# Optimization experiments

Measured on AMD Instinct MI355X. Metric: run time of the kernel, lower is better.

Reference implementation:

```python
import jax, jax.numpy as jnp
import numpy as np

B, D, L = 4096, 128, 4
ALPHA = 1.0
SLOPE = 0.1  # LeakyReLU negative slope


def _leaky(h):
    return jnp.where(h > 0, h, SLOPE * h)


def _dleaky(h):
    return jnp.where(h > 0, 1.0, SLOPE).astype(h.dtype)


def setup_inputs() -> dict:
    key = jax.random.key(0)
    ks = jax.random.split(key, 7)
    scale = 0.5 / np.sqrt(D)  # keep residual roughly Lipschitz < 1
    x = jax.random.normal(ks[0], (B, D), jnp.float32)
    W1 = jax.random.normal(ks[1], (L, D, D), jnp.float32) * scale
    b1 = jax.random.normal(ks[2], (L, D), jnp.float32) * 0.01
    W2 = jax.random.normal(ks[3], (L, D, D), jnp.float32) * scale
    b2 = jax.random.normal(ks[4], (L, D), jnp.float32) * 0.01
    W3 = jax.random.normal(ks[5], (L, D, D), jnp.float32) * scale
    b3 = jax.random.normal(ks[6], (L, D), jnp.float32) * 0.01
    return {"x": x, "W1": W1, "b1": b1, "W2": W2, "b2": b2, "W3": W3, "b3": b3}


def reference(x, W1, b1, W2, b2, W3, b3):
    logdet = jnp.zeros(x.shape[0], x.dtype)
    for i in range(L):  # small fixed number of structurally distinct blocks
        w1, w2, w3 = W1[i], W2[i], W3[i]
        # --- block forward: x <- x + alpha * f(x) ---
        h1 = x @ w1.T + b1[i]
        h2 = _leaky(h1) @ w2.T + b2[i]
        f = _leaky(h2) @ w3.T + b3[i]
        x = x + ALPHA * f
        # --- log|det J_f| evaluated at the NEW x (as in the original code) ---
        g1 = x @ w1.T + b1[i]          # [B, D] pre-activation 1
        d1 = _dleaky(g1)
        g2 = _leaky(g1) @ w2.T + b2[i]  # [B, D] pre-activation 2
        d2 = _dleaky(g2)
        # J[b] = w3 @ diag(d2[b]) @ w2 @ diag(d1[b]) @ w1  -> [B, D, D]
        J = (w3[None, :, :] * d2[:, None, :]) @ w2
        J = (J * d1[:, None, :]) @ w1
        s = jnp.linalg.svd(J, compute_uv=False)  # [B, D] singular values
        logdet = logdet + jnp.sum(jnp.log(s), axis=-1)
    return x, logdet
```

## Files before the change

kernel.cpp:

```cpp
#include <hip/hip_runtime.h>

typedef __attribute__((ext_vector_type(8))) short short8;
typedef __attribute__((ext_vector_type(4))) float float4f;

#define PITCH 136
#define ROWS 32
#define LOG_SLOPE -2.302585092994046f
#define LN2 0.6931471805599453f
#define NBLK 140
#define LDS_BYTES 69760
#define WS_BIAS 4160
#define WS_WPLANES 8192
#define NWELEM 196608

__device__ __forceinline__ float bf2f(unsigned int u) {
    return __builtin_bit_cast(float, u << 16);
}
__device__ __forceinline__ unsigned short f2bf(float f) {
    unsigned int x = __builtin_bit_cast(unsigned int, f);
    x += 0x7fff + ((x >> 16) & 1);
    return (unsigned short)(x >> 16);
}
__device__ __forceinline__ float4f vmsub(float4f a, float s, float4f b) {
    a[0] -= s * b[0]; a[1] -= s * b[1]; a[2] -= s * b[2]; a[3] -= s * b[3];
    return a;
}

template<int ISF32>
__device__ __forceinline__ float ldv(const void* p, int i) {
    if (ISF32) return ((const float*)p)[i];
    return bf2f(((const unsigned short*)p)[i]);
}

__device__ __forceinline__ int detect_f32(const unsigned short* W1u, int lane) {
    unsigned int u = W1u[lane * 2];
    unsigned int e = (u >> 7) & 0xFF;
    int bad = (e < 64) || (e > 135);
    return __ballot(bad) != 0ull;
}

__device__ __forceinline__ float4f mfma16(short8 a, short8 b, float4f c) {
    return __builtin_amdgcn_mfma_f32_16x16x32_bf16(a, b, c, 0, 0, 0);
}

__device__ __forceinline__ void split8(float4f a, float4f b, short8& hi, short8& lo) {
#pragma unroll
    for (int j = 0; j < 4; ++j) {
        float v = a[j]; unsigned short h = f2bf(v);
        hi[j] = (short)h; lo[j] = (short)f2bf(v - bf2f(h));
        v = b[j]; h = f2bf(v);
        hi[4 + j] = (short)h; lo[4 + j] = (short)f2bf(v - bf2f(h));
    }
}

__global__ void k_prep(const void* __restrict__ W1, const void* __restrict__ W2,
                       const void* __restrict__ W3, const void* __restrict__ b1,
                       const void* __restrict__ b2, const void* __restrict__ b3,
                       float* __restrict__ ws) {
    const int tid = threadIdx.x, bid = blockIdx.x;
    const int isf32 = detect_f32((const unsigned short*)W1, tid & 63);
    unsigned short* whi = (unsigned short*)(ws + WS_WPLANES);
    unsigned short* wlo = whi + NWELEM;
    if (bid < 96) {
        int s = (bid * 256 + tid) * 8;
        int mat = s >> 14, off = s & 16383;
        int wsel = mat >> 2;
        const void* Wm = wsel == 0 ? W1 : (wsel == 1 ? W2 : W3);
        int src = (mat & 3) * 16384 + off;
        short8 hi, lo;
        if (isf32) {
            const float* p = (const float*)Wm + src;
            split8(*(const float4f*)p, *(const float4f*)(p + 4), hi, lo);
        } else {
            hi = *(const short8*)((const unsigned short*)Wm + src);
            lo = (short8){0, 0, 0, 0, 0, 0, 0, 0};
        }
        *(short8*)(whi + s) = hi;
        *(short8*)(wlo + s) = lo;
    } else {
        for (int e = tid; e < 1536; e += 256) {
            int bsel = e >> 9, idx = e & 511;
            const void* bp = bsel == 0 ? b1 : (bsel == 1 ? b2 : b3);
            ws[WS_BIAS + e] = isf32 ? ((const float*)bp)[idx]
                                    : bf2f(((const unsigned short*)bp)[idx]);
        }
        if (tid == 0) ((int*)ws)[0] = 0;
    }
}

struct W8 { short8 v[16]; };

__device__ __forceinline__ W8 loadW(const unsigned short* __restrict__ wh,
                                    const unsigned short* __restrict__ wl,
                                    int c0, int c1, int q) {
    W8 r;
#pragma unroll
    for (int kk = 0; kk < 4; ++kk) {
        const int kc = kk * 32 + q * 8;
        r.v[kk * 4 + 0] = *(const short8*)(wh + c0 * 128 + kc);
        r.v[kk * 4 + 1] = *(const short8*)(wh + c1 * 128 + kc);
        r.v[kk * 4 + 2] = *(const short8*)(wl + c0 * 128 + kc);
        r.v[kk * 4 + 3] = *(const short8*)(wl + c1 * 128 + kc);
    }
    return r;
}

template<int MODE>
__device__ __forceinline__ W8 matvec(const W8& w,
        const unsigned short* inh, const unsigned short* inl,
        unsigned short* outh, unsigned short* outl,
        const unsigned short* resh, const unsigned short* resl,
        const unsigned short* __restrict__ nwh, const unsigned short* __restrict__ nwl,
        const float* __restrict__ bias,
        int lane, int colb, int* cnt) {
    const int m = lane & 15, q = lane >> 4;
    const int c0 = colb + m, c1 = colb + 16 + m;
    float b0 = bias[c0], b1v = bias[c1];
    float4f acc[2][2];
#pragma unroll
    for (int rt = 0; rt < 2; ++rt) {
        acc[rt][0] = (float4f){b0, b0, b0, b0};
        acc[rt][1] = (float4f){b1v, b1v, b1v, b1v};
    }
    __syncthreads();
    W8 wn = loadW(nwh, nwl, c0, c1, q);
#pragma unroll
    for (int kk = 0; kk < 4; ++kk) {
        const int kc = kk * 32 + q * 8;
#pragma unroll
        for (int rt = 0; rt < 2; ++rt) {
            short8 xh = *(const short8*)(inh + (rt * 16 + m) * PITCH + kc);
            short8 xl = *(const short8*)(inl + (rt * 16 + m) * PITCH + kc);
            acc[rt][0] = mfma16(xh, w.v[kk * 4 + 0], acc[rt][0]);
            acc[rt][0] = mfma16(xl, w.v[kk * 4 + 0], acc[rt][0]);
            acc[rt][0] = mfma16(xh, w.v[kk * 4 + 2], acc[rt][0]);
            acc[rt][1] = mfma16(xh, w.v[kk * 4 + 1], acc[rt][1]);
            acc[rt][1] = mfma16(xl, w.v[kk * 4 + 1], acc[rt][1]);
            acc[rt][1] = mfma16(xh, w.v[kk * 4 + 3], acc[rt][1]);
        }
    }
    int c[2][4];
#pragma unroll
    for (int rt = 0; rt < 2; ++rt) {
#pragma unroll
        for (int r = 0; r < 4; ++r) {
            float v0 = acc[rt][0][r], v1 = acc[rt][1][r];
            int row = rt * 16 + q * 4 + r;
            int o0 = row * PITCH + c0, o1 = row * PITCH + c1;
            if (MODE == 1) {
                v0 += bf2f(resh[o0]) + bf2f(resl[o0]);
                v1 += bf2f(resh[o1]) + bf2f(resl[o1]);
            }
            if (MODE >= 2) c[rt][r] = (v0 <= 0.0f) + (v1 <= 0.0f);
            if (MODE == 0 || MODE == 2) {
                v0 = v0 > 0.0f ? v0 : 0.1f * v0;
                v1 = v1 > 0.0f ? v1 : 0.1f * v1;
            }
            if (MODE != 3) {
                unsigned short h0 = f2bf(v0);
                outh[o0] = h0; outl[o0] = f2bf(v0 - bf2f(h0));
                unsigned short h1 = f2bf(v1);
                outh[o1] = h1; outl[o1] = f2bf(v1 - bf2f(h1));
            }
        }
    }
    if (MODE >= 2) {
#pragma unroll
        for (int rt = 0; rt < 2; ++rt) {
#pragma unroll
            for (int r = 0; r < 4; ++r) {
                int cc = c[rt][r];
                cc += __shfl_xor(cc, 1);
                cc += __shfl_xor(cc, 2);
                cc += __shfl_xor(cc, 4);
                cc += __shfl_xor(cc, 8);
                if (m == 0) atomicAdd(&cnt[rt * 16 + q * 4 + r], cc);
            }
        }
    }
    return wn;
}

template<int ISF32>
__device__ __forceinline__ void fwd(int bid, int tid, int lane, char* ldsb,
                                    const void* x, const float* ws, void* out,
                                    float* wsw) {
    unsigned short* P = (unsigned short*)ldsb;
    unsigned short* Ah = P;
    unsigned short* Al = P + 1 * ROWS * PITCH;
    unsigned short* Bh = P + 2 * ROWS * PITCH;
    unsigned short* Bl = P + 3 * ROWS * PITCH;
    unsigned short* Th = P + 4 * ROWS * PITCH;
    unsigned short* Tl = P + 5 * ROWS * PITCH;
    unsigned short* Uh = P + 6 * ROWS * PITCH;
    unsigned short* Ul = P + 7 * ROWS * PITCH;
    int* cnt = (int*)(P + 8 * ROWS * PITCH);
    const unsigned short* whi = (const unsigned short*)(ws + WS_WPLANES);
    const unsigned short* wlo = whi + NWELEM;
    const float* bias = ws + WS_BIAS;
    const int r0 = bid * ROWS;
    const int m = lane & 15, q = lane >> 4;
    const int colb = (tid >> 6) * 32;
    const int c0 = colb + m, c1 = colb + 16 + m;
    W8 wcur = loadW(whi, wlo, c0, c1, q);
    for (int e = tid; e < ROWS * 128; e += 256) {
        int r = e >> 7, c = e & 127;
        float v = ldv<ISF32>(x, (r0 + r) * 128 + c);
        unsigned short h = f2bf(v);
        Ah[r * PITCH + c] = h;
        Al[r * PITCH + c] = f2bf(v - bf2f(h));
    }
    if (tid < ROWS) cnt[tid] = 0;
    unsigned short *curh = Ah, *curl = Al, *othh = Bh, *othl = Bl;
#pragma unroll 1
    for (int layer = 0; layer < 4; ++layer) {
        const unsigned short* w1h = whi + (0 + layer) * 16384;
        const unsigned short* w1l = wlo + (0 + layer) * 16384;
        const unsigned short* w2h = whi + (4 + layer) * 16384;
        const unsigned short* w2l = wlo + (4 + layer) * 16384;
        const unsigned short* w3h = whi + (8 + layer) * 16384;
        const unsigned short* w3l = wlo + (8 + layer) * 16384;
        const unsigned short* n1h = whi + ((layer + 1) & 3) * 16384;
        const unsigned short* n1l = wlo + ((layer + 1) & 3) * 16384;
        const float* b1p = bias + layer * 128;
        const float* b2p = bias + 512 + layer * 128;
        const float* b3p = bias + 1024 + layer * 128;
        wcur = matvec<0>(wcur, curh, curl, Th, Tl, 0, 0, w2h, w2l, b1p, lane, colb, cnt);
        wcur = matvec<0>(wcur, Th, Tl, Uh, Ul, 0, 0, w3h, w3l, b2p, lane, colb, cnt);
        wcur = matvec<1>(wcur, Uh, Ul, othh, othl, curh, curl, w1h, w1l, b3p, lane, colb, cnt);
        wcur = matvec<2>(wcur, othh, othl, Th, Tl, 0, 0, w2h, w2l, b1p, lane, colb, cnt);
        wcur = matvec<3>(wcur, Th, Tl, Th, Tl, 0, 0, n1h, n1l, b2p, lane, colb, cnt);
        unsigned short* t;
        t = curh; curh = othh; othh = t;
        t = curl; curl = othl; othl = t;
    }
    __syncthreads();
    for (int e = tid; e < ROWS * 128; e += 256) {
        int r = e >> 7, c = e & 127;
        float v = bf2f(curh[r * PITCH + c]) + bf2f(curl[r * PITCH + c]);
        if (ISF32) ((float*)out)[(r0 + r) * 128 + c] = v;
        else ((unsigned short*)out)[(r0 + r) * 128 + c] = f2bf(v);
    }
    if (tid < ROWS) wsw[64 + r0 + tid] = (float)cnt[tid];
}

template<int ISF32>
__device__ __forceinline__ float lu_logdet(int id, int tid, float* lds,
        const void* W1, const void* W2, const void* W3) {
    const int wsel = id % 3;
    const void* Wm = (wsel == 0 ? W1 : (wsel == 1 ? W2 : W3));
    const int ofs = (id / 3) * 16384;
    const int tx = tid & 31, ty = tid >> 5;
    float* rowbuf = lds;
    float* colbuf = lds + 1024;
    float4f V[16];
#pragma unroll
    for (int m = 0; m < 16; ++m) {
        int base = ofs + (ty + 8 * m) * 128 + 4 * tx;
        if (ISF32) {
            V[m] = *(const float4f*)((const float*)Wm + base);
        } else {
            ushort4 u = *(const ushort4*)((const unsigned short*)Wm + base);
            V[m] = (float4f){bf2f(u.x), bf2f(u.y), bf2f(u.z), bf2f(u.w)};
        }
    }
    if (ty < 4) *(float4f*)&rowbuf[ty * 128 + 4 * tx] = V[0];
    if (tx == 0) {
#pragma unroll
        for (int j = 0; j < 4; ++j) {
#pragma unroll
            for (int mg = 0; mg < 4; ++mg) {
                float4f t = {V[mg * 4 + 0][j], V[mg * 4 + 1][j],
                             V[mg * 4 + 2][j], V[mg * 4 + 3][j]};
                *(float4f*)&colbuf[j * 128 + ty * 16 + mg * 4] = t;
            }
        }
    }
    __syncthreads();
    float logacc = 0.0f;
#pragma unroll 1
    for (int kap = 0; kap < 32; ++kap) {
        const int K = kap * 4;
        const int buf = (kap & 1) * 512;
        float4f D[4], R[4], C[4][4];
#pragma unroll
        for (int j = 0; j < 4; ++j) {
            D[j] = *(const float4f*)&rowbuf[buf + j * 128 + K];
            R[j] = *(const float4f*)&rowbuf[buf + j * 128 + 4 * tx];
#pragma unroll
            for (int mg = 0; mg < 4; ++mg)
                C[j][mg] = *(const float4f*)&colbuf[buf + j * 128 + ty * 16 + mg * 4];
        }
        float p0 = D[0][0], i0 = 1.0f / p0;
        float l10 = D[1][0] * i0, l20 = D[2][0] * i0, l30 = D[3][0] * i0;
        D[1] = vmsub(D[1], l10, D[0]); R[1] = vmsub(R[1], l10, R[0]);
        D[2] = vmsub(D[2], l20, D[0]); R[2] = vmsub(R[2], l20, R[0]);
        D[3] = vmsub(D[3], l30, D[0]); R[3] = vmsub(R[3], l30, R[0]);
        float p1 = D[1][1], i1 = 1.0f / p1;
        float l21 = D[2][1] * i1, l31 = D[3][1] * i1;
        D[2] = vmsub(D[2], l21, D[1]); R[2] = vmsub(R[2], l21, R[1]);
        D[3] = vmsub(D[3], l31, D[1]); R[3] = vmsub(R[3], l31, R[1]);
        float p2 = D[2][2], i2 = 1.0f / p2;
        float l32 = D[3][2] * i2;
        D[3] = vmsub(D[3], l32, D[2]); R[3] = vmsub(R[3], l32, R[2]);
        float p3 = D[3][3], i3 = 1.0f / p3;
        logacc += __log2f(fabsf(p0)) + __log2f(fabsf(p1))
                + __log2f(fabsf(p2)) + __log2f(fabsf(p3));
        float iv[4] = {i0, i1, i2, i3};
#pragma unroll
        for (int i = 0; i < 4; ++i) {
#pragma unroll
            for (int mg = 0; mg < 4; ++mg) {
#pragma unroll
                for (int e = 0; e < 4; ++e) {
                    int r = ty + 32 * mg + 8 * e;
                    C[i][mg][e] = (r > K + i) ? C[i][mg][e] * iv[i] : 0.0f;
                }
            }
#pragma unroll
            for (int j = i + 1; j < 4; ++j) {
                float uij = D[i][j];
#pragma unroll
                for (int mg = 0; mg < 4; ++mg)
                    C[j][mg] = vmsub(C[j][mg], uij, C[i][mg]);
            }
        }
#pragma unroll
        for (int mg = 0; mg < 4; ++mg) {
#pragma unroll
            for (int e = 0; e < 4; ++e) {
                float4f v = V[mg * 4 + e];
                v = vmsub(v, C[0][mg][e], R[0]);
                v = vmsub(v, C[1][mg][e], R[1]);
                v = vmsub(v, C[2][mg][e], R[2]);
                v = vmsub(v, C[3][mg][e], R[3]);
                V[mg * 4 + e] = v;
            }
        }
        if (kap < 31) {
            const int nbuf = ((kap + 1) & 1) * 512;
            const int tb = (kap & 1) ? 0 : 4;
            const int mn = (kap + 1) >> 1;
            if (ty >= tb && ty < tb + 4) {
                float4f val;
                switch (mn) {
                case 0:  val = V[0];  break; case 1:  val = V[1];  break;
                case 2:  val = V[2];  break; case 3:  val = V[3];  break;
                case 4:  val = V[4];  break; case 5:  val = V[5];  break;
                case 6:  val = V[6];  break; case 7:  val = V[7];  break;
                case 8:  val = V[8];  break; case 9:  val = V[9];  break;
                case 10: val = V[10]; break; case 11: val = V[11]; break;
                case 12: val = V[12]; break; case 13: val = V[13]; break;
                case 14: val = V[14]; break; default: val = V[15]; break;
                }
                *(float4f*)&rowbuf[nbuf + (ty - tb) * 128 + 4 * tx] = val;
            }
            if (tx == kap + 1) {
#pragma unroll
                for (int j = 0; j < 4; ++j) {
#pragma unroll
                    for (int mg = 0; mg < 4; ++mg) {
                        float4f t = {V[mg * 4 + 0][j], V[mg * 4 + 1][j],
                                     V[mg * 4 + 2][j], V[mg * 4 + 3][j]};
                        *(float4f*)&colbuf[nbuf + j * 128 + ty * 16 + mg * 4] = t;
                    }
                }
            }
        }
        __syncthreads();
    }
    return logacc * LN2;
}

__global__ __launch_bounds__(256) void k_main(
        const void* __restrict__ x,
        const void* __restrict__ W1, const void* __restrict__ b1,
        const void* __restrict__ W2, const void* __restrict__ b2,
        const void* __restrict__ W3, const void* __restrict__ b3,
        void* __restrict__ out, float* __restrict__ ws) {
    extern __shared__ __align__(16) char ldsb[];
    __shared__ int s_last;
    const int tid = threadIdx.x;
    const int lane = tid & 63;
    const int isf32 = detect_f32((const unsigned short*)W1, lane);

    if (blockIdx.x < 12) {
        float ld = isf32 ? lu_logdet<1>(blockIdx.x, tid, (float*)ldsb, W1, W2, W3)
                         : lu_logdet<0>(blockIdx.x, tid, (float*)ldsb, W1, W2, W3);
        if (tid == 0) ws[2 + blockIdx.x] = ld;
    } else {
        const int bid = blockIdx.x - 12;
        if (isf32) fwd<1>(bid, tid, lane, ldsb, x, ws, out, ws);
        else       fwd<0>(bid, tid, lane, ldsb, x, ws, out, ws);
    }

    __threadfence();
    if (tid == 0) s_last = (atomicAdd((int*)ws, 1) == NBLK - 1);
    __syncthreads();
    if (!s_last) return;
    __threadfence();
    float s = 0.0f;
#pragma unroll
    for (int i = 0; i < 12; ++i) s += ws[2 + i];
    for (int b = tid; b < 4096; b += 256) {
        float v = s + LOG_SLOPE * ws[64 + b];
        if (isf32) ((float*)out)[524288 + b] = v;
        else ((unsigned short*)out)[524288 + b] = f2bf(v);
    }
}

extern "C" void kernel_launch(void* const* d_in, const int* in_sizes, int n_in,
                              void* d_out, int out_size, void* d_ws, size_t ws_size,
                              hipStream_t stream) {
    const void* x  = d_in[0];
    const void* W1 = d_in[1];
    const void* b1 = d_in[2];
    const void* W2 = d_in[3];
    const void* b2 = d_in[4];
    const void* W3 = d_in[5];
    const void* b3 = d_in[6];
    float* ws = (float*)d_ws;

    hipLaunchKernelGGL(k_prep, dim3(97), dim3(256), 0, stream,
                       W1, W2, W3, b1, b2, b3, ws);
    hipLaunchKernelGGL(k_main, dim3(NBLK), dim3(256), LDS_BYTES, stream,
                       x, W1, b1, W2, b2, W3, b3, d_out, ws);
}
```

Baseline: 136.6 us.

## Restructure forward pass to one wave per 16-row block with register-resident weights

Each forward block now runs a single 64-lane wave over 16 rows instead of four waves over 32 rows. That wave computes all 128 output columns, streaming weight tiles through a 32-entry register buffer, and keeps the fp32 residual in registers. This removes per-matvec __syncthreads, the LDS residual reads and the shared-memory atomics for the negative-count, and raises the block count so more CUs are busy. The cost is heavier register pressure per wave and serial weight-tile loads inside each matvec. Extra threads in forward blocks exit early while the 256-thread launch is kept.

```diff
diff --git a/kernel.cpp b/kernel.cpp
--- a/kernel.cpp
+++ b/kernel.cpp
@@ -4,11 +4,10 @@
 typedef __attribute__((ext_vector_type(4))) float float4f;
 
 #define PITCH 136
-#define ROWS 32
 #define LOG_SLOPE -2.302585092994046f
 #define LN2 0.6931471805599453f
-#define NBLK 140
-#define LDS_BYTES 69760
+#define NBLK 268
+#define LDS_BYTES 26112
 #define WS_BIAS 4160
 #define WS_WPLANES 8192
 #define NWELEM 196608
@@ -88,130 +87,117 @@
     }
 }
 
-struct W8 { short8 v[16]; };
-
-__device__ __forceinline__ W8 loadW(const unsigned short* __restrict__ wh,
-                                    const unsigned short* __restrict__ wl,
-                                    int c0, int c1, int q) {
-    W8 r;
+__device__ __forceinline__ void loadTile(short8* d,
+                                         const unsigned short* __restrict__ wh,
+                                         const unsigned short* __restrict__ wl,
+                                         int ct, int m, int q) {
+    const unsigned short* ph = wh + (ct * 16 + m) * 128 + q * 8;
+    const unsigned short* pl = wl + (ct * 16 + m) * 128 + q * 8;
 #pragma unroll
     for (int kk = 0; kk < 4; ++kk) {
-        const int kc = kk * 32 + q * 8;
-        r.v[kk * 4 + 0] = *(const short8*)(wh + c0 * 128 + kc);
-        r.v[kk * 4 + 1] = *(const short8*)(wh + c1 * 128 + kc);
-        r.v[kk * 4 + 2] = *(const short8*)(wl + c0 * 128 + kc);
-        r.v[kk * 4 + 3] = *(const short8*)(wl + c1 * 128 + kc);
-    }
-    return r;
+        d[kk * 2 + 0] = *(const short8*)(ph + kk * 32);
+        d[kk * 2 + 1] = *(const short8*)(pl + kk * 32);
+    }
 }
 
 template<int MODE>
-__device__ __forceinline__ W8 matvec(const W8& w,
-        const unsigned short* inh, const unsigned short* inl,
+__device__ __forceinline__ void matvec(
+        const unsigned short* __restrict__ inh, const unsigned short* __restrict__ inl,
         unsigned short* outh, unsigned short* outl,
-        const unsigned short* resh, const unsigned short* resl,
+        const unsigned short* __restrict__ cwh, const unsigned short* __restrict__ cwl,
         const unsigned short* __restrict__ nwh, const unsigned short* __restrict__ nwl,
         const float* __restrict__ bias,
-        int lane, int colb, int* cnt) {
-    const int m = lane & 15, q = lane >> 4;
-    const int c0 = colb + m, c1 = colb + 16 + m;
-    float b0 = bias[c0], b1v = bias[c1];
-    float4f acc[2][2];
-#pragma unroll
-    for (int rt = 0; rt < 2; ++rt) {
-        acc[rt][0] = (float4f){b0, b0, b0, b0};
-        acc[rt][1] = (float4f){b1v, b1v, b1v, b1v};
-    }
-    __syncthreads();
-    W8 wn = loadW(nwh, nwl, c0, c1, q);
+        float4f* res, int* cnt, short8* Wb, int m, int q) {
+    short8 xh[4], xl[4];
 #pragma unroll
     for (int kk = 0; kk < 4; ++kk) {
-        const int kc = kk * 32 + q * 8;
-#pragma unroll
-        for (int rt = 0; rt < 2; ++rt) {
-            short8 xh = *(const short8*)(inh + (rt * 16 + m) * PITCH + kc);
-            short8 xl = *(const short8*)(inl + (rt * 16 + m) * PITCH + kc);
-            acc[rt][0] = mfma16(xh, w.v[kk * 4 + 0], acc[rt][0]);
-            acc[rt][0] = mfma16(xl, w.v[kk * 4 + 0], acc[rt][0]);
-            acc[rt][0] = mfma16(xh, w.v[kk * 4 + 2], acc[rt][0]);
-            acc[rt][1] = mfma16(xh, w.v[kk * 4 + 1], acc[rt][1]);
-            acc[rt][1] = mfma16(xl, w.v[kk * 4 + 1], acc[rt][1]);
-            acc[rt][1] = mfma16(xh, w.v[kk * 4 + 3], acc[rt][1]);
-        }
-    }
-    int c[2][4];
-#pragma unroll
-    for (int rt = 0; rt < 2; ++rt) {
+        xh[kk] = *(const short8*)(inh + m * PITCH + kk * 32 + q * 8);
+        xl[kk] = *(const short8*)(inl + m * PITCH + kk * 32 + q * 8);
+    }
+    float bv[8];
+#pragma unroll
+    for (int ct = 0; ct < 8; ++ct) bv[ct] = bias[ct * 16 + m];
+    float4f acc[8];
+#pragma unroll
+    for (int ct = 0; ct < 8; ++ct) acc[ct] = (float4f){0.f, 0.f, 0.f, 0.f};
+#pragma unroll
+    for (int p = 0; p < 4; ++p) {
+        const int t0 = 2 * p, t1 = 2 * p + 1;
+        const int s0 = (p & 1) * 16, s1 = s0 + 8;
+#pragma unroll
+        for (int kk = 0; kk < 4; ++kk) {
+            acc[t0] = mfma16(xh[kk], Wb[s0 + kk * 2 + 0], acc[t0]);
+            acc[t1] = mfma16(xh[kk], Wb[s1 + kk * 2 + 0], acc[t1]);
+            acc[t0] = mfma16(xl[kk], Wb[s0 + kk * 2 + 0], acc[t0]);
+            acc[t1] = mfma16(xl[kk], Wb[s1 + kk * 2 + 0], acc[t1]);
+            acc[t0] = mfma16(xh[kk], Wb[s0 + kk * 2 + 1], acc[t0]);
+            acc[t1] = mfma16(xh[kk], Wb[s1 + kk * 2 + 1], acc[t1]);
+        }
+        if (p < 2) {
+            loadTile(Wb + s0, cwh, cwl, t0 + 4, m, q);
+            loadTile(Wb + s1, cwh, cwl, t1 + 4, m, q);
+        } else {
+            loadTile(Wb + s0, nwh, nwl, t0 - 4, m, q);
+            loadTile(Wb + s1, nwh, nwl, t1 - 4, m, q);
+        }
+    }
+#pragma unroll
+    for (int ct = 0; ct < 8; ++ct) {
 #pragma unroll
         for (int r = 0; r < 4; ++r) {
-            float v0 = acc[rt][0][r], v1 = acc[rt][1][r];
-            int row = rt * 16 + q * 4 + r;
-            int o0 = row * PITCH + c0, o1 = row * PITCH + c1;
-            if (MODE == 1) {
-                v0 += bf2f(resh[o0]) + bf2f(resl[o0]);
-                v1 += bf2f(resh[o1]) + bf2f(resl[o1]);
-            }
-            if (MODE >= 2) c[rt][r] = (v0 <= 0.0f) + (v1 <= 0.0f);
-            if (MODE == 0 || MODE == 2) {
-                v0 = v0 > 0.0f ? v0 : 0.1f * v0;
-                v1 = v1 > 0.0f ? v1 : 0.1f * v1;
-            }
+            float v = acc[ct][r] + bv[ct];
+            if (MODE >= 2) cnt[r] += (v <= 0.0f) ? 1 : 0;
+            if (MODE == 0 || MODE == 2) v = fmaxf(v, 0.1f * v);
+            if (MODE == 1) { v += res[ct * 1][r]; res[ct][r] = v; }
             if (MODE != 3) {
-                unsigned short h0 = f2bf(v0);
-                outh[o0] = h0; outl[o0] = f2bf(v0 - bf2f(h0));
-                unsigned short h1 = f2bf(v1);
-                outh[o1] = h1; outl[o1] = f2bf(v1 - bf2f(h1));
-            }
-        }
-    }
-    if (MODE >= 2) {
-#pragma unroll
-        for (int rt = 0; rt < 2; ++rt) {
-#pragma unroll
-            for (int r = 0; r < 4; ++r) {
-                int cc = c[rt][r];
-                cc += __shfl_xor(cc, 1);
-                cc += __shfl_xor(cc, 2);
-                cc += __shfl_xor(cc, 4);
-                cc += __shfl_xor(cc, 8);
-                if (m == 0) atomicAdd(&cnt[rt * 16 + q * 4 + r], cc);
-            }
-        }
-    }
-    return wn;
+                const int o = (q * 4 + r) * PITCH + ct * 16 + m;
+                unsigned short h = f2bf(v);
+                outh[o] = h;
+                outl[o] = f2bf(v - bf2f(h));
+            }
+        }
+    }
 }
 
 template<int ISF32>
-__device__ __forceinline__ void fwd(int bid, int tid, int lane, char* ldsb,
-                                    const void* x, const float* ws, void* out,
-                                    float* wsw) {
+__device__ void fwd(int bid, int lane, char* ldsb,
+                    const void* __restrict__ x, const float* __restrict__ ws,
+                    void* __restrict__ out, float* __restrict__ wsw) {
     unsigned short* P = (unsigned short*)ldsb;
-    unsigned short* Ah = P;
-    unsigned short* Al = P + 1 * ROWS * PITCH;
-    unsigned short* Bh = P + 2 * ROWS * PITCH;
-    unsigned short* Bl = P + 3 * ROWS * PITCH;
-    unsigned short* Th = P + 4 * ROWS * PITCH;
-    unsigned short* Tl = P + 5 * ROWS * PITCH;
-    unsigned short* Uh = P + 6 * ROWS * PITCH;
-    unsigned short* Ul = P + 7 * ROWS * PITCH;
-    int* cnt = (int*)(P + 8 * ROWS * PITCH);
+    unsigned short* P0h = P + 0 * 16 * PITCH;
+    unsigned short* P0l = P + 1 * 16 * PITCH;
+    unsigned short* P1h = P + 2 * 16 * PITCH;
+    unsigned short* P1l = P + 3 * 16 * PITCH;
+    unsigned short* P2h = P + 4 * 16 * PITCH;
+    unsigned short* P2l = P + 5 * 16 * PITCH;
     const unsigned short* whi = (const unsigned short*)(ws + WS_WPLANES);
     const unsigned short* wlo = whi + NWELEM;
     const float* bias = ws + WS_BIAS;
-    const int r0 = bid * ROWS;
+    const int r0 = bid * 16;
     const int m = lane & 15, q = lane >> 4;
-    const int colb = (tid >> 6) * 32;
-    const int c0 = colb + m, c1 = colb + 16 + m;
-    W8 wcur = loadW(whi, wlo, c0, c1, q);
-    for (int e = tid; e < ROWS * 128; e += 256) {
+
+    short8 Wb[32];
+    loadTile(Wb + 0,  whi, wlo, 0, m, q);
+    loadTile(Wb + 8,  whi, wlo, 1, m, q);
+    loadTile(Wb + 16, whi, wlo, 2, m, q);
+    loadTile(Wb + 24, whi, wlo, 3, m, q);
+
+    float4f res[8];
+#pragma unroll
+    for (int ct = 0; ct < 8; ++ct) {
+#pragma unroll
+        for (int r = 0; r < 4; ++r)
+            res[ct][r] = ldv<ISF32>(x, (r0 + q * 4 + r) * 128 + ct * 16 + m);
+    }
+#pragma unroll 4
+    for (int e = lane; e < 2048; e += 64) {
         int r = e >> 7, c = e & 127;
         float v = ldv<ISF32>(x, (r0 + r) * 128 + c);
         unsigned short h = f2bf(v);
-        Ah[r * PITCH + c] = h;
-        Al[r * PITCH + c] = f2bf(v - bf2f(h));
-    }
-    if (tid < ROWS) cnt[tid] = 0;
-    unsigned short *curh = Ah, *curl = Al, *othh = Bh, *othl = Bl;
+        P0h[r * PITCH + c] = h;
+        P0l[r * PITCH + c] = f2bf(v - bf2f(h));
+    }
+    int cnt[4] = {0, 0, 0, 0};
 #pragma unroll 1
     for (int layer = 0; layer < 4; ++layer) {
         const unsigned short* w1h = whi + (0 + layer) * 16384;
@@ -225,23 +211,31 @@
         const float* b1p = bias + layer * 128;
         const float* b2p = bias + 512 + layer * 128;
         const float* b3p = bias + 1024 + layer * 128;
-        wcur = matvec<0>(wcur, curh, curl, Th, Tl, 0, 0, w2h, w2l, b1p, lane, colb, cnt);
-        wcur = matvec<0>(wcur, Th, Tl, Uh, Ul, 0, 0, w3h, w3l, b2p, lane, colb, cnt);
-        wcur = matvec<1>(wcur, Uh, Ul, othh, othl, curh, curl, w1h, w1l, b3p, lane, colb, cnt);
-        wcur = matvec<2>(wcur, othh, othl, Th, Tl, 0, 0, w2h, w2l, b1p, lane, colb, cnt);
-        wcur = matvec<3>(wcur, Th, Tl, Th, Tl, 0, 0, n1h, n1l, b2p, lane, colb, cnt);
-        unsigned short* t;
-        t = curh; curh = othh; othh = t;
-        t = curl; curl = othl; othl = t;
-    }
-    __syncthreads();
-    for (int e = tid; e < ROWS * 128; e += 256) {
-        int r = e >> 7, c = e & 127;
-        float v = bf2f(curh[r * PITCH + c]) + bf2f(curl[r * PITCH + c]);
-        if (ISF32) ((float*)out)[(r0 + r) * 128 + c] = v;
-        else ((unsigned short*)out)[(r0 + r) * 128 + c] = f2bf(v);
-    }
-    if (tid < ROWS) wsw[64 + r0 + tid] = (float)cnt[tid];
+        matvec<0>(P0h, P0l, P1h, P1l, w1h, w1l, w2h, w2l, b1p, res, cnt, Wb, m, q);
+        matvec<0>(P1h, P1l, P2h, P2l, w2h, w2l, w3h, w3l, b2p, res, cnt, Wb, m, q);
+        matvec<1>(P2h, P2l, P0h, P0l, w3h, w3l, w1h, w1l, b3p, res, cnt, Wb, m, q);
+        matvec<2>(P0h, P0l, P1h, P1l, w1h, w1l, w2h, w2l, b1p, res, cnt, Wb, m, q);
+        matvec<3>(P1h, P1l, P1h, P1l, w2h, w2l, n1h, n1l, b2p, res, cnt, Wb, m, q);
+    }
+#pragma unroll
+    for (int r = 0; r < 4; ++r) {
+        int c = cnt[r];
+        c += __shfl_xor(c, 1);
+        c += __shfl_xor(c, 2);
+        c += __shfl_xor(c, 4);
+        c += __shfl_xor(c, 8);
+        if (m == 0) wsw[64 + r0 + q * 4 + r] = (float)c;
+    }
+#pragma unroll
+    for (int ct = 0; ct < 8; ++ct) {
+#pragma unroll
+        for (int r = 0; r < 4; ++r) {
+            float v = res[ct][r];
+            const int o = (r0 + q * 4 + r) * 128 + ct * 16 + m;
+            if (ISF32) ((float*)out)[o] = v;
+            else ((unsigned short*)out)[o] = f2bf(v);
+        }
+    }
 }
 
 template<int ISF32>
@@ -372,37 +366,39 @@
     return logacc * LN2;
 }
 
-__global__ __launch_bounds__(256) void k_main(
+__global__ __launch_bounds__(256, 1) void k_main(
         const void* __restrict__ x,
         const void* __restrict__ W1, const void* __restrict__ b1,
         const void* __restrict__ W2, const void* __restrict__ b2,
         const void* __restrict__ W3, const void* __restrict__ b3,
         void* __restrict__ out, float* __restrict__ ws) {
     extern __shared__ __align__(16) char ldsb[];
-    __shared__ int s_last;
     const int tid = threadIdx.x;
     const int lane = tid & 63;
+    if (blockIdx.x >= 12 && tid >= 64) return;
     const int isf32 = detect_f32((const unsigned short*)W1, lane);
 
     if (blockIdx.x < 12) {
         float ld = isf32 ? lu_logdet<1>(blockIdx.x, tid, (float*)ldsb, W1, W2, W3)
                          : lu_logdet<0>(blockIdx.x, tid, (float*)ldsb, W1, W2, W3);
         if (tid == 0) ws[2 + blockIdx.x] = ld;
+        if (tid >= 64) return;
     } else {
         const int bid = blockIdx.x - 12;
-        if (isf32) fwd<1>(bid, tid, lane, ldsb, x, ws, out, ws);
-        else       fwd<0>(bid, tid, lane, ldsb, x, ws, out, ws);
+        if (isf32) fwd<1>(bid, lane, ldsb, x, ws, out, ws);
+        else       fwd<0>(bid, lane, ldsb, x, ws, out, ws);
     }
 
     __threadfence();
-    if (tid == 0) s_last = (atomicAdd((int*)ws, 1) == NBLK - 1);
-    __syncthreads();
-    if (!s_last) return;
+    int lastf = 0;
+    if (lane == 0) lastf = (atomicAdd((int*)ws, 1) == NBLK - 1) ? 1 : 0;
+    lastf = __shfl(lastf, 0);
+    if (!lastf) return;
     __threadfence();
     float s = 0.0f;
 #pragma unroll
     for (int i = 0; i < 12; ++i) s += ws[2 + i];
-    for (int b = tid; b < 4096; b += 256) {
+    for (int b = lane; b < 4096; b += 64) {
         float v = s + LOG_SLOPE * ws[64 + b];
         if (isf32) ((float*)out)[524288 + b] = v;
         else ((unsigned short*)out)[524288 + b] = f2bf(v);
```

Result: slower. 253.0 us (+85.3%).
